# Optimization experiments

Hardware: AMD Instinct MI355X
Metric: run time of the kernel (lower is better)

## Reference

```python
import jax, jax.numpy as jnp
import numpy as np

TEMP = 0.07
BASE_TEMP = 0.07
EPS = 1e-12


def setup_inputs() -> dict:
    key = jax.random.key(0)
    k1, k2, k3 = jax.random.split(key, 3)
    B, V, D, C = 4096, 1, 128, 100
    features = jax.random.normal(k1, (B, V, D), dtype=jnp.float32)
    labels = jax.random.randint(k2, (B,), 0, C, dtype=jnp.int64)
    covariances = jax.random.normal(k3, (C, D, D), dtype=jnp.float32)
    return {"features": features, "labels": labels, "covariances": covariances}


def reference(features, labels, covariances):
    B, n_views = features.shape[0], features.shape[1]
    feats = features.reshape(B, n_views, -1)
    # cat(unbind(dim=1), dim=0); with n_views==1 this is feats[:, 0]
    contrast_feature = jnp.concatenate([feats[:, v] for v in range(n_views)], axis=0)
    anchor_feature = contrast_feature  # contrast_mode == 'all'

    # mask_{i,j} = 1 if labels match
    mask = (labels[:, None] == labels[None, :]).astype(jnp.float32)  # [B,B]

    similarity_matrix = anchor_feature @ contrast_feature.T  # [B,B]

    # dis[i,j] = a_i^T C_{label_i} a_j  (gather cov per anchor, one bilinear form per pair)
    cov_g = covariances[labels]                              # [B,D,D] irregular gather
    v = jnp.einsum('id,ide->ie', anchor_feature, cov_g)      # [B,D]
    dis_matrix = v @ anchor_feature.T                        # [B,B]

    logits = (similarity_matrix + dis_matrix / (2.0 * TEMP ** 2)) / TEMP
    logits = logits - jax.lax.stop_gradient(jnp.max(logits, axis=1, keepdims=True))
    log_prob = logits - jnp.log(jnp.sum(jnp.exp(logits), axis=1, keepdims=True) + EPS)

    # original: (mask[:,:,None] * log_prob).sum(1) == mask @ log_prob (avoids B^3 temp)
    mask_sum = mask.sum(axis=1, keepdims=True)               # [B,1]
    mean_log_prob_pos = (mask @ log_prob) / (mask_sum + EPS)  # [B,B]
    loss = -(TEMP / BASE_TEMP) * mean_log_prob_pos
    return loss.mean()
```

## Files before the change

kernel.cpp:

```cpp
#include <hip/hip_runtime.h>
#include <hip/hip_bf16.h>


#define DIM 128
#define TEMP 0.07f

typedef __attribute__((ext_vector_type(8))) short short8;
typedef __attribute__((ext_vector_type(4))) float floatx4;

static __device__ __forceinline__ unsigned short f2bf(float f) {
    __hip_bfloat16 h = __float2bfloat16(f);
    union { __hip_bfloat16 h; unsigned short u; } c;
    c.h = h;
    return c.u;
}

__global__ __launch_bounds__(256) void prep_kernel(
    const float* __restrict__ A, const int* __restrict__ labels,
    const float* __restrict__ Cov, unsigned short* __restrict__ Wbf,
    unsigned short* __restrict__ Abf) {
    const float inv2t2 = 1.0f / (2.0f * TEMP * TEMP);
    const float invt = 1.0f / TEMP;
    const int sub = threadIdx.x >> 7;
    const int e = threadIdx.x & 127;
    const int i = blockIdx.x * 2 + sub;
    __shared__ float a[2][DIM];
    float av = A[(size_t)i * DIM + e];
    a[sub][e] = av;
    Abf[(size_t)i * DIM + e] = f2bf(av);
    __syncthreads();
    int c = labels[i];
    const float* Cp = Cov + (size_t)c * (DIM * DIM) + e;
    float acc = 0.0f;
#pragma unroll 8
    for (int d = 0; d < DIM; ++d) {
        acc = fmaf(a[sub][d], Cp[(size_t)d * DIM], acc);
    }
    Wbf[(size_t)i * DIM + e] = f2bf((av + acc * inv2t2) * invt);
}

__global__ __launch_bounds__(256, 2) void main_kernel(
    const unsigned short* __restrict__ Wbf, const unsigned short* __restrict__ Abf,
    float* __restrict__ mP, float* __restrict__ zP, float* __restrict__ sP,
    int Jsplit, int JSWEEP, int nP) {
    __shared__ __align__(16) unsigned short sW[128 * 128];
    __shared__ __align__(16) unsigned short sA[64 * 128];

    const int mb = blockIdx.x / Jsplit;
    const int jsp = blockIdx.x % Jsplit;
    const int rowBase = mb * 128;
    const int t = threadIdx.x;
    const int wave = t >> 6, lane = t & 63, quad = lane >> 4, l16 = lane & 15;
    const int waveM = wave >> 1, waveN = wave & 1;

    {
        int row = t >> 1, half = t & 1, rsw = row & 15;
        const unsigned short* src = Wbf + (size_t)(rowBase + row) * DIM + half * 64;
        unsigned short* dstrow = sW + row * 128;
#pragma unroll
        for (int i = 0; i < 8; i++) {
            int c = half * 8 + i;
            *(short8*)(dstrow + ((c ^ rsw) << 3)) = *(const short8*)(src + i * 8);
        }
    }

    float run_m[4][4], run_Z[4][4], run_s[4][4];
#pragma unroll
    for (int a = 0; a < 4; a++)
#pragma unroll
        for (int r = 0; r < 4; r++) {
            run_m[a][r] = -3.4e38f; run_Z[a][r] = 0.f; run_s[a][r] = 0.f;
        }

    const int arow = t >> 2, aq = t & 3, arsw = arow & 15;
    const unsigned short* asrc0 =
        Abf + (size_t)(jsp * JSWEEP * 64 + arow) * DIM + aq * 32;
    unsigned short* adst = sA + arow * 128;

    short8 pre[4];
#pragma unroll
    for (int i = 0; i < 4; i++) pre[i] = *(const short8*)(asrc0 + i * 8);

    const unsigned short* myW = sW + (size_t)(waveM * 64 + l16) * 128;
    const unsigned short* myA = sA + (size_t)(waveN * 32 + l16) * 128;

    for (int js = 0; js < JSWEEP; ++js) {
        __syncthreads();
#pragma unroll
        for (int i = 0; i < 4; i++) {
            int c = aq * 4 + i;
            *(short8*)(adst + ((c ^ arsw) << 3)) = pre[i];
        }
        __syncthreads();

        if (js + 1 < JSWEEP) {
            const unsigned short* nsrc = asrc0 + (size_t)(js + 1) * 64 * DIM;
#pragma unroll
            for (int i = 0; i < 4; i++) pre[i] = *(const short8*)(nsrc + i * 8);
        }

        floatx4 acc[4][2];
#pragma unroll
        for (int mt = 0; mt < 4; mt++)
#pragma unroll
            for (int nt = 0; nt < 2; nt++) acc[mt][nt] = (floatx4)0.f;

#pragma unroll
        for (int kst = 0; kst < 4; ++kst) {
            const int coff = (((kst << 2) | quad) ^ l16) << 3;
            short8 bfrag[2];
#pragma unroll
            for (int nt = 0; nt < 2; nt++)
                bfrag[nt] = *(const short8*)(myA + nt * 16 * 128 + coff);
#pragma unroll
            for (int mt = 0; mt < 4; mt++) {
                short8 afrag = *(const short8*)(myW + mt * 16 * 128 + coff);
#pragma unroll
                for (int nt = 0; nt < 2; nt++)
                    acc[mt][nt] = __builtin_amdgcn_mfma_f32_16x16x32_bf16(
                        afrag, bfrag[nt], acc[mt][nt], 0, 0, 0);
            }
        }

#pragma unroll
        for (int mt = 0; mt < 4; mt++)
#pragma unroll
            for (int r = 0; r < 4; r++) {
                float v0 = acc[mt][0][r], v1 = acc[mt][1][r];
                float tm = fmaxf(v0, v1);
                float nm = fmaxf(run_m[mt][r], tm);
                run_Z[mt][r] = run_Z[mt][r] * __expf(run_m[mt][r] - nm)
                             + __expf(v0 - nm) + __expf(v1 - nm);
                run_m[mt][r] = nm;
                run_s[mt][r] += v0 + v1;
            }
    }

    const int chunk = jsp * 2 + waveN;
#pragma unroll
    for (int mt = 0; mt < 4; mt++)
#pragma unroll
        for (int r = 0; r < 4; r++) {
            float m = run_m[mt][r], Z = run_Z[mt][r], s = run_s[mt][r];
#pragma unroll
            for (int mask = 1; mask < 16; mask <<= 1) {
                float om = __shfl_xor(m, mask);
                float oZ = __shfl_xor(Z, mask);
                float os = __shfl_xor(s, mask);
                float nm = fmaxf(m, om);
                Z = Z * __expf(m - nm) + oZ * __expf(om - nm);
                m = nm;
                s += os;
            }
            if (l16 == r) {
                int row = rowBase + waveM * 64 + mt * 16 + quad * 4 + r;
                size_t idx = (size_t)row * nP + chunk;
                mP[idx] = m; zP[idx] = Z; sP[idx] = s;
            }
        }
}

__global__ __launch_bounds__(64) void combine_kernel(
    const float* __restrict__ mP, const float* __restrict__ zP,
    const float* __restrict__ sP, double* __restrict__ Sk, int B, int nP) {
    int k = blockIdx.x;
    int l = threadIdx.x;
    float m = -3.4e38f, Z = 0.0f, s = 0.0f;
    if (l < nP) {
        size_t idx = (size_t)k * nP + l;
        m = mP[idx]; Z = zP[idx]; s = sP[idx];
    }
    float M = m;
#pragma unroll
    for (int o = 32; o > 0; o >>= 1) M = fmaxf(M, __shfl_xor(M, o));
    float zt = Z * __expf(m - M);
    float st = s;
#pragma unroll
    for (int o = 32; o > 0; o >>= 1) {
        zt += __shfl_xor(zt, o);
        st += __shfl_xor(st, o);
    }
    if (l == 0) {
        Sk[k] = (double)st - (double)B * (double)M
                - (double)B * log((double)zt + 1e-12);
    }
}

__global__ __launch_bounds__(1024) void final_kernel(
    const double* __restrict__ Sk, const int* __restrict__ labels,
    float* __restrict__ out, int B) {
    __shared__ int hist[128];
    __shared__ double sh[1024];
    int t = threadIdx.x;
    if (t < 128) hist[t] = 0;
    __syncthreads();
    for (int i = t; i < B; i += 1024) atomicAdd(&hist[labels[i]], 1);
    __syncthreads();
    double acc = 0.0;
    for (int i = t; i < B; i += 1024) {
        double cnt = (double)hist[labels[i]];
        acc += Sk[i] * (cnt / (cnt + 1e-12));
    }
    sh[t] = acc;
    __syncthreads();
    for (int o = 512; o > 0; o >>= 1) {
        if (t < o) sh[t] += sh[t + o];
        __syncthreads();
    }
    if (t == 0) out[0] = (float)(-sh[0] / ((double)B * (double)B));
}

extern "C" void kernel_launch(void* const* d_in, const int* in_sizes, int n_in,
                              void* d_out, int out_size, void* d_ws, size_t ws_size,
                              hipStream_t stream) {
    const float* A = (const float*)d_in[0];
    const int* labels = (const int*)d_in[1];
    const float* Cov = (const float*)d_in[2];
    float* out = (float*)d_out;

    int B = in_sizes[0] / DIM;
    int Jsplit = 16;
    int JSWEEP = B / (Jsplit * 64);
    int nP = Jsplit * 2;

    char* ws = (char*)d_ws;
    unsigned short* Wbf = (unsigned short*)ws;
    unsigned short* Abf = Wbf + (size_t)B * DIM;
    float* mP = (float*)(Abf + (size_t)B * DIM);
    float* zP = mP + (size_t)B * nP;
    float* sP = zP + (size_t)B * nP;
    double* Sk = (double*)(sP + (size_t)B * nP);

    prep_kernel<<<B / 2, 256, 0, stream>>>(A, labels, Cov, Wbf, Abf);
    main_kernel<<<(B / 128) * Jsplit, 256, 0, stream>>>(Wbf, Abf, mP, zP, sP,
                                                        Jsplit, JSWEEP, nP);
    combine_kernel<<<B, 64, 0, stream>>>(mP, zP, sP, Sk, B, nP);
    final_kernel<<<1, 1024, 0, stream>>>(Sk, labels, out, B);
}
```

Before: 100.7 us.

## Bucket rows by label so prep reuses each covariance load across 16 rows

Adds a single-block bucketing kernel that sorts row indices by class and splits each class into chunks of up to 16 rows. The prep kernel then processes one chunk per block, so each covariance element loaded from global memory feeds 8 FMAs (one per row a thread handles) instead of one. Before, every row streamed its own 64KB covariance matrix. The cost is an extra serial single-block kernel launch, a gather through perm, and per-class chunk imbalance, in exchange for much less covariance traffic in prep.

Measured after the change: 125.5 us. 24.6% more time.

```diff
diff --git a/kernel.cpp b/kernel.cpp
--- a/kernel.cpp
+++ b/kernel.cpp
@@ -4,6 +4,9 @@
 
 #define DIM 128
 #define TEMP 0.07f
+#define NBIN 128
+#define CHUNK 16
+#define MAXCHUNK 512
 
 typedef __attribute__((ext_vector_type(8))) short short8;
 typedef __attribute__((ext_vector_type(4))) float floatx4;
@@ -15,28 +18,96 @@
     return c.u;
 }
 
+__global__ __launch_bounds__(1024) void bucket_kernel(
+    const int* __restrict__ labels, int B, int* __restrict__ perm,
+    int* __restrict__ ckCls, int* __restrict__ ckBase,
+    int* __restrict__ ckNv, int* __restrict__ meta) {
+    __shared__ int cnt[NBIN], pos[NBIN];
+    const int t = threadIdx.x;
+    if (t < NBIN) cnt[t] = 0;
+    __syncthreads();
+    for (int i = t; i < B; i += 1024) atomicAdd(&cnt[labels[i]], 1);
+    __syncthreads();
+    if (t == 0) {
+        int run = 0, ci = 0;
+        for (int c = 0; c < NBIN; ++c) {
+            const int n = cnt[c];
+            pos[c] = run;
+            for (int j = 0; j < n; j += CHUNK) {
+                ckCls[ci] = c;
+                ckBase[ci] = run + j;
+                ckNv[ci] = (n - j < CHUNK) ? (n - j) : CHUNK;
+                ++ci;
+            }
+            run += n;
+        }
+        meta[0] = ci;
+    }
+    __syncthreads();
+    for (int i = t; i < B; i += 1024) {
+        const int c = labels[i];
+        const int p = atomicAdd(&pos[c], 1);
+        perm[p] = i;
+    }
+    if (t < NBIN) meta[1 + t] = cnt[t];
+}
+
 __global__ __launch_bounds__(256) void prep_kernel(
-    const float* __restrict__ A, const int* __restrict__ labels,
-    const float* __restrict__ Cov, unsigned short* __restrict__ Wbf,
-    unsigned short* __restrict__ Abf) {
+    const float* __restrict__ A, const float* __restrict__ Cov,
+    unsigned short* __restrict__ Wbf, unsigned short* __restrict__ Abf,
+    const int* __restrict__ perm, const int* __restrict__ ckCls,
+    const int* __restrict__ ckBase, const int* __restrict__ ckNv,
+    const int* __restrict__ meta) {
     const float inv2t2 = 1.0f / (2.0f * TEMP * TEMP);
     const float invt = 1.0f / TEMP;
-    const int sub = threadIdx.x >> 7;
-    const int e = threadIdx.x & 127;
-    const int i = blockIdx.x * 2 + sub;
-    __shared__ float a[2][DIM];
-    float av = A[(size_t)i * DIM + e];
-    a[sub][e] = av;
-    Abf[(size_t)i * DIM + e] = f2bf(av);
-    __syncthreads();
-    int c = labels[i];
-    const float* Cp = Cov + (size_t)c * (DIM * DIM) + e;
-    float acc = 0.0f;
+    __shared__ float a_t[DIM][CHUNK];
+    __shared__ int rowids[CHUNK];
+    const int b = blockIdx.x;
+    if (b >= meta[0]) return;
+    const int cls = ckCls[b], base = ckBase[b], nv = ckNv[b];
+    const int t = threadIdx.x;
+    {
+        const int k = t >> 4, j = t & 15;
+        const int row = perm[base + (k < nv ? k : 0)];
+        if (j == 0) rowids[k] = row;
+        const float4 v0 = *(const float4*)(A + (size_t)row * DIM + j * 8);
+        const float4 v1 = *(const float4*)(A + (size_t)row * DIM + j * 8 + 4);
+        const float va[8] = {v0.x, v0.y, v0.z, v0.w, v1.x, v1.y, v1.z, v1.w};
+        short8 ab;
+#pragma unroll
+        for (int i = 0; i < 8; ++i) {
+            a_t[j * 8 + i][k] = va[i];
+            ab[i] = (short)f2bf(va[i]);
+        }
+        if (k < nv) *(short8*)(Abf + (size_t)row * DIM + j * 8) = ab;
+    }
+    __syncthreads();
+    const int e = t & 127, half = t >> 7;
+    const float* Cp = Cov + (size_t)cls * (DIM * DIM) + e;
+    float acc[8] = {0.f, 0.f, 0.f, 0.f, 0.f, 0.f, 0.f, 0.f};
 #pragma unroll 8
     for (int d = 0; d < DIM; ++d) {
-        acc = fmaf(a[sub][d], Cp[(size_t)d * DIM], acc);
-    }
-    Wbf[(size_t)i * DIM + e] = f2bf((av + acc * inv2t2) * invt);
+        const float cov = Cp[(size_t)d * DIM];
+        const float4 w0 = *(const float4*)&a_t[d][half * 8];
+        const float4 w1 = *(const float4*)&a_t[d][half * 8 + 4];
+        acc[0] = fmaf(w0.x, cov, acc[0]);
+        acc[1] = fmaf(w0.y, cov, acc[1]);
+        acc[2] = fmaf(w0.z, cov, acc[2]);
+        acc[3] = fmaf(w0.w, cov, acc[3]);
+        acc[4] = fmaf(w1.x, cov, acc[4]);
+        acc[5] = fmaf(w1.y, cov, acc[5]);
+        acc[6] = fmaf(w1.z, cov, acc[6]);
+        acc[7] = fmaf(w1.w, cov, acc[7]);
+    }
+#pragma unroll
+    for (int kk = 0; kk < 8; ++kk) {
+        const int krow = half * 8 + kk;
+        if (krow < nv) {
+            const int row = rowids[krow];
+            const float av = A[(size_t)row * DIM + e];
+            Wbf[(size_t)row * DIM + e] = f2bf((av + acc[kk] * inv2t2) * invt);
+        }
+    }
 }
 
 __global__ __launch_bounds__(256, 2) void main_kernel(
@@ -188,13 +259,11 @@
 
 __global__ __launch_bounds__(1024) void final_kernel(
     const double* __restrict__ Sk, const int* __restrict__ labels,
-    float* __restrict__ out, int B) {
-    __shared__ int hist[128];
+    const int* __restrict__ cntG, float* __restrict__ out, int B) {
+    __shared__ int hist[NBIN];
     __shared__ double sh[1024];
     int t = threadIdx.x;
-    if (t < 128) hist[t] = 0;
-    __syncthreads();
-    for (int i = t; i < B; i += 1024) atomicAdd(&hist[labels[i]], 1);
+    if (t < NBIN) hist[t] = cntG[t];
     __syncthreads();
     double acc = 0.0;
     for (int i = t; i < B; i += 1024) {
@@ -230,10 +299,18 @@
     float* zP = mP + (size_t)B * nP;
     float* sP = zP + (size_t)B * nP;
     double* Sk = (double*)(sP + (size_t)B * nP);
-
-    prep_kernel<<<B / 2, 256, 0, stream>>>(A, labels, Cov, Wbf, Abf);
+    int* perm = (int*)(Sk + B);
+    int* ckCls = perm + B;
+    int* ckBase = ckCls + MAXCHUNK;
+    int* ckNv = ckBase + MAXCHUNK;
+    int* meta = ckNv + MAXCHUNK;
+
+    bucket_kernel<<<1, 1024, 0, stream>>>(labels, B, perm, ckCls, ckBase,
+                                          ckNv, meta);
+    prep_kernel<<<MAXCHUNK, 256, 0, stream>>>(A, Cov, Wbf, Abf, perm, ckCls,
+                                              ckBase, ckNv, meta);
     main_kernel<<<(B / 128) * Jsplit, 256, 0, stream>>>(Wbf, Abf, mP, zP, sP,
                                                         Jsplit, JSWEEP, nP);
     combine_kernel<<<B, 64, 0, stream>>>(mP, zP, sP, Sk, B, nP);
-    final_kernel<<<1, 1024, 0, stream>>>(Sk, labels, out, B);
-}
+    final_kernel<<<1, 1024, 0, stream>>>(Sk, labels, meta + 1, out, B);
+}
```
